# Performance work log

Measured on AMD Instinct MI355X. Metric: run time of the kernel, lower is better.

## Reference

```python
import jax, jax.numpy as jnp
import numpy as np

N = 100000   # nodes
E = 1600000  # edges (avg degree 16)
G = 512      # graphs in batch
IN = 96      # in_channels
H = 128      # hidden_channels
C = 100      # num_classes
ED = 8       # edge_dim
L = 4        # num_layers
EPS_LN = 1e-5


def setup_inputs() -> dict:
    key = jax.random.key(0)
    ks = jax.random.split(key, 24)
    s = 0.05
    d = {
        "x": jax.random.normal(ks[0], (N, IN), jnp.float32),
        "edge_index": jax.random.randint(ks[1], (2, E), 0, N, jnp.int32),
        "batch": jnp.sort(jax.random.randint(ks[2], (N,), 0, G, jnp.int32)),
        "edge_attr": jax.random.normal(ks[3], (E, ED), jnp.float32),
        # edge encoder MLP: Linear(ED,H) -> ReLU -> Linear(H,1)
        "ee_W1": jax.random.normal(ks[4], (ED, H), jnp.float32) * s,
        "ee_b1": jnp.zeros((H,), jnp.float32),
        "ee_W2": jax.random.normal(ks[5], (H, 1), jnp.float32) * s,
        "ee_b2": jnp.zeros((1,), jnp.float32),
        # GCNConv weights (PyG: lin without bias, bias added after aggregation)
        "W0": jax.random.normal(ks[6], (IN, H), jnp.float32) * s,
        "cb0": jnp.zeros((H,), jnp.float32),
        "W1": jax.random.normal(ks[7], (H, H), jnp.float32) * s,
        "cb1": jnp.zeros((H,), jnp.float32),
        "W2": jax.random.normal(ks[8], (H, H), jnp.float32) * s,
        "cb2": jnp.zeros((H,), jnp.float32),
        "W3": jax.random.normal(ks[9], (H, H), jnp.float32) * s,
        "cb3": jnp.zeros((H,), jnp.float32),
        # LayerNorm params
        "g0": jnp.ones((H,), jnp.float32), "be0": jnp.zeros((H,), jnp.float32),
        "g1": jnp.ones((H,), jnp.float32), "be1": jnp.zeros((H,), jnp.float32),
        "g2": jnp.ones((H,), jnp.float32), "be2": jnp.zeros((H,), jnp.float32),
        "g3": jnp.ones((H,), jnp.float32), "be3": jnp.zeros((H,), jnp.float32),
        # residual projection for layer 0 only (IN != H)
        "res_W": jax.random.normal(ks[10], (IN, H), jnp.float32) * s,
        "res_b": jnp.zeros((H,), jnp.float32),
        # head: Linear(2H,H) -> ReLU -> Linear(H,C)
        "hW1": jax.random.normal(ks[11], (2 * H, H), jnp.float32) * s,
        "hb1": jnp.zeros((H,), jnp.float32),
        "hW2": jax.random.normal(ks[12], (H, C), jnp.float32) * s,
        "hb2": jnp.zeros((C,), jnp.float32),
    }
    return d


def _layer_norm(h, g, b):
    mu = jnp.mean(h, axis=-1, keepdims=True)
    var = jnp.mean(jnp.square(h - mu), axis=-1, keepdims=True)
    return g * (h - mu) / jnp.sqrt(var + EPS_LN) + b


def reference(x, edge_index, batch, edge_attr,
              ee_W1, ee_b1, ee_W2, ee_b2,
              W0, cb0, W1, cb1, W2, cb2, W3, cb3,
              g0, be0, g1, be1, g2, be2, g3, be3,
              res_W, res_b, hW1, hb1, hW2, hb2):
    row, col = edge_index[0], edge_index[1]

    # edge weight = softplus(MLP(edge_attr)) + 1e-4  -> [E]
    eh = jax.nn.relu(edge_attr @ ee_W1 + ee_b1)
    ew = jax.nn.softplus((eh @ ee_W2 + ee_b2)[:, 0]) + 1e-4

    # add self loops with weight 1 (PyG GCNConv default)
    loops = jnp.arange(N, dtype=row.dtype)
    row_sl = jnp.concatenate([row, loops])
    col_sl = jnp.concatenate([col, loops])
    ew_sl = jnp.concatenate([ew, jnp.ones((N,), ew.dtype)])

    # symmetric normalization: D^-1/2 A D^-1/2 (deg over target index)
    deg = jax.ops.segment_sum(ew_sl, col_sl, num_segments=N)
    dis = jnp.where(deg > 0, jax.lax.rsqrt(deg), 0.0)
    norm = dis[row_sl] * ew_sl * dis[col_sl]  # [E+N]

    def conv(h, W, b):
        hw = h @ W                                   # [N,H]
        msg = hw[row_sl] * norm[:, None]             # [E+N,H]
        return jax.ops.segment_sum(msg, col_sl, num_segments=N) + b

    Ws = [W0, W1, W2, W3]
    cbs = [cb0, cb1, cb2, cb3]
    gs = [g0, g1, g2, g3]
    bes = [be0, be1, be2, be3]

    hidden = []
    cur = x
    for i in range(L):
        h = conv(cur, Ws[i], cbs[i])
        h = _layer_norm(h, gs[i], bes[i])
        res = cur @ res_W + res_b if i == 0 else cur
        h = jax.nn.relu(h + res)
        # dropout: eval mode -> identity
        hidden.append(h)
        cur = h
    xm = jnp.mean(jnp.stack(hidden, axis=0), axis=0)  # [N,H]

    # meanmax pooling over graphs
    counts = jax.ops.segment_sum(jnp.ones((N,), xm.dtype), batch, num_segments=G)
    gmean = jax.ops.segment_sum(xm, batch, num_segments=G) / jnp.maximum(counts, 1.0)[:, None]
    gmax = jax.ops.segment_max(xm, batch, num_segments=G)
    gmax = jnp.where(jnp.isfinite(gmax), gmax, 0.0)
    g = jnp.concatenate([gmean, gmax], axis=-1)       # [G,2H]

    # head (dropout identity in eval)
    return jax.nn.relu(g @ hW1 + hb1) @ hW2 + hb2     # [G,C]
```

## Files before the change

kernel.cpp:

```cpp
#include <hip/hip_runtime.h>
#include <hip/hip_fp16.h>
#include <math.h>

#define NN 100000
#define EE 1600000
#define GB 512
#define INC 96
#define HH 128
#define CC 100
#define MAXD 64

typedef __bf16 bf16x8 __attribute__((ext_vector_type(8)));
typedef _Float16 f16x8 __attribute__((ext_vector_type(8)));
typedef float f32x4 __attribute__((ext_vector_type(4)));

__global__ __launch_bounds__(256) void k_cast(const float* __restrict__ src, __half* __restrict__ dst, int n4) {
    int i = blockIdx.x * 256 + threadIdx.x;
    if (i >= n4) return;
    float4 v = *(const float4*)&src[(size_t)i * 4];
    __half2 a = __floats2half2_rn(v.x, v.y);
    __half2 b = __floats2half2_rn(v.z, v.w);
    *(__half2*)&dst[(size_t)i * 4]     = a;
    *(__half2*)&dst[(size_t)i * 4 + 2] = b;
}

__global__ __launch_bounds__(256) void k_castT(const float* __restrict__ W, __half* __restrict__ Wt, int K) {
    int idx = blockIdx.x * 256 + threadIdx.x;
    if (idx >= K * 128) return;
    int k = idx >> 7, n = idx & 127;
    Wt[(size_t)n * K + k] = __float2half(W[idx]);
}

__global__ __launch_bounds__(512) void k_prep_w1(const float* __restrict__ W1, __bf16* __restrict__ w1f) {
    int tid = threadIdx.x;
    int t = tid >> 6, lane = tid & 63;
    int ln15 = lane & 15, quad = lane >> 4;
    bf16x8 v = {};
    if (quad == 0) {
#pragma unroll
        for (int j = 0; j < 8; ++j) v[j] = (__bf16)W1[j * 128 + t * 16 + ln15];
    }
    *(bf16x8*)&w1f[(size_t)(t * 64 + lane) * 8] = v;
}

__global__ __launch_bounds__(256) void k_edge_mlp_mfma(
    const float* __restrict__ ea,
    const __bf16* __restrict__ w1f, const float* __restrict__ b1,
    const float* __restrict__ W2, const float* __restrict__ b2,
    float* __restrict__ ew)
{
    __shared__ float sDot[128];
    int tid = threadIdx.x, wv = tid >> 6, lane = tid & 63;
    int ln15 = lane & 15, quad = lane >> 4;
    int ebase = blockIdx.x * 128 + wv * 32;

    bf16x8 bfr[8];
#pragma unroll
    for (int t = 0; t < 8; ++t) bfr[t] = *(const bf16x8*)&w1f[(size_t)(t * 64 + lane) * 8];

    bf16x8 a0 = {}, a1 = {};
    if (quad == 0) {
        const float* p0 = &ea[(size_t)(ebase + ln15) * 8];
        float4 u0 = *(const float4*)p0, u1 = *(const float4*)(p0 + 4);
        a0[0] = (__bf16)u0.x; a0[1] = (__bf16)u0.y; a0[2] = (__bf16)u0.z; a0[3] = (__bf16)u0.w;
        a0[4] = (__bf16)u1.x; a0[5] = (__bf16)u1.y; a0[6] = (__bf16)u1.z; a0[7] = (__bf16)u1.w;
        const float* p1 = &ea[(size_t)(ebase + 16 + ln15) * 8];
        float4 w0 = *(const float4*)p1, w1v = *(const float4*)(p1 + 4);
        a1[0] = (__bf16)w0.x; a1[1] = (__bf16)w0.y; a1[2] = (__bf16)w0.z; a1[3] = (__bf16)w0.w;
        a1[4] = (__bf16)w1v.x; a1[5] = (__bf16)w1v.y; a1[6] = (__bf16)w1v.z; a1[7] = (__bf16)w1v.w;
    }

    f32x4 d0 = {0.f, 0.f, 0.f, 0.f}, d1 = {0.f, 0.f, 0.f, 0.f};
#pragma unroll
    for (int t = 0; t < 8; ++t) {
        f32x4 z = {0.f, 0.f, 0.f, 0.f};
        f32x4 c0 = __builtin_amdgcn_mfma_f32_16x16x32_bf16(a0, bfr[t], z, 0, 0, 0);
        f32x4 c1 = __builtin_amdgcn_mfma_f32_16x16x32_bf16(a1, bfr[t], z, 0, 0, 0);
        int col = t * 16 + ln15;
        float b1v = b1[col], w2v = W2[col];
#pragma unroll
        for (int r = 0; r < 4; ++r) {
            float v0 = fmaxf(c0[r] + b1v, 0.0f);
            float v1 = fmaxf(c1[r] + b1v, 0.0f);
            d0[r] = fmaf(v0, w2v, d0[r]);
            d1[r] = fmaf(v1, w2v, d1[r]);
        }
    }
#pragma unroll
    for (int o = 1; o < 16; o <<= 1) {
#pragma unroll
        for (int r = 0; r < 4; ++r) {
            d0[r] += __shfl_xor(d0[r], o, 64);
            d1[r] += __shfl_xor(d1[r], o, 64);
        }
    }
    if (ln15 == 0) {
#pragma unroll
        for (int r = 0; r < 4; ++r) {
            sDot[wv * 32 + quad * 4 + r]      = d0[r];
            sDot[wv * 32 + 16 + quad * 4 + r] = d1[r];
        }
    }
    __syncthreads();
    if (tid < 128) {
        int e = blockIdx.x * 128 + tid;
        float x = sDot[tid] + b2[0];
        float sp = (x > 20.0f) ? x : log1pf(expf(x));
        ew[e] = sp + 1e-4f;
    }
}

__global__ __launch_bounds__(256) void k_scatter(const int* __restrict__ ei, const float* __restrict__ ew,
                                                 int* __restrict__ cnt, int2* __restrict__ epack, int E) {
    int e = blockIdx.x * 256 + threadIdx.x;
    if (e >= E) return;
    int r = ei[e], c = ei[E + e];
    float w = ew[e];
    int rank = atomicAdd(&cnt[c], 1);
    if (rank < MAXD) epack[(size_t)c * MAXD + rank] = make_int2(r, __float_as_int(w));
}

__global__ __launch_bounds__(256) void k_degk(int* __restrict__ cnt, const int2* __restrict__ epack,
                                              float* __restrict__ dis, int n) {
    int i = blockIdx.x * 256 + threadIdx.x;
    if (i >= n) return;
    int c = cnt[i]; c = c < MAXD ? c : MAXD;
    cnt[i] = c;
    const int2* base = &epack[(size_t)i * MAXD];
    float d = 1.0f;
    for (int k = 0; k < c; ++k) d += __int_as_float(base[k].y);
    dis[i] = rsqrtf(d);
}

__global__ __launch_bounds__(256) void k_norm(const int* __restrict__ cnt, const float* __restrict__ dis,
                                              int2* __restrict__ epack, int n) {
    int wv = threadIdx.x >> 6, lane = threadIdx.x & 63;
    int i = blockIdx.x * 4 + wv;
    if (i >= n) return;
    float dc = dis[i];
    if (lane < cnt[i]) {
        int2 e = epack[(size_t)i * MAXD + lane];
        float wn = dis[e.x] * __int_as_float(e.y) * dc;
        __half h = __float2half(wn);
        __half2 p = __halves2half2(h, h);
        union { __half2 h2; int i32; } u; u.h2 = p;
        epack[(size_t)i * MAXD + lane].y = u.i32;
    }
}

__global__ __launch_bounds__(256) void k_gemm_f16(
    const __half* __restrict__ A, const __half* __restrict__ Bt,
    const float* __restrict__ bias, __half* __restrict__ C, int M, int K)
{
    int tid = threadIdx.x;
    int wv = tid >> 6, lane = tid & 63;
    int ln15 = lane & 15, quad = lane >> 4;
    int m0 = blockIdx.x * 64;
    int n0 = wv * 32;
    f32x4 acc[4][2];
#pragma unroll
    for (int mt = 0; mt < 4; ++mt)
#pragma unroll
        for (int nt = 0; nt < 2; ++nt) acc[mt][nt] = (f32x4){0.f, 0.f, 0.f, 0.f};

    int rowm[4];
#pragma unroll
    for (int mt = 0; mt < 4; ++mt) {
        int r = m0 + mt * 16 + ln15;
        rowm[mt] = r < M ? r : M - 1;
    }
    for (int kc = 0; kc < K; kc += 32) {
        f16x8 af[4], bfr[2];
#pragma unroll
        for (int mt = 0; mt < 4; ++mt)
            af[mt] = *(const f16x8*)&A[(size_t)rowm[mt] * K + kc + quad * 8];
#pragma unroll
        for (int nt = 0; nt < 2; ++nt)
            bfr[nt] = *(const f16x8*)&Bt[(size_t)(n0 + nt * 16 + ln15) * K + kc + quad * 8];
#pragma unroll
        for (int mt = 0; mt < 4; ++mt)
#pragma unroll
            for (int nt = 0; nt < 2; ++nt)
                acc[mt][nt] = __builtin_amdgcn_mfma_f32_16x16x32_f16(af[mt], bfr[nt], acc[mt][nt], 0, 0, 0);
    }
#pragma unroll
    for (int nt = 0; nt < 2; ++nt) {
        int col = n0 + nt * 16 + ln15;
        float bv = bias ? bias[col] : 0.0f;
#pragma unroll
        for (int mt = 0; mt < 4; ++mt) {
#pragma unroll
            for (int r = 0; r < 4; ++r) {
                int row = m0 + mt * 16 + quad * 4 + r;
                if (row < M) C[(size_t)row * 128 + col] = __float2half(acc[mt][nt][r] + bv);
            }
        }
    }
}

__global__ __launch_bounds__(256) void k_agg_ln(
    const __half* __restrict__ hw, const float* __restrict__ dis,
    const int* __restrict__ cnt, const int2* __restrict__ epack,
    const float* __restrict__ cb, const float* __restrict__ gam,
    const float* __restrict__ bet, const __half* __restrict__ res,
    __half* __restrict__ out, int n)
{
    int wv = threadIdx.x >> 6;
    int lane = threadIdx.x & 63;
    int i = blockIdx.x * 4 + wv;
    if (i >= n) return;
    float di = dis[i];
    float sn = di * di;
    __half2 own = *(const __half2*)&hw[(size_t)i * HH + lane * 2];
    __half hsn = __float2half(sn);
    __half2 acc = __hmul2(own, __halves2half2(hsn, hsn));
    int cn = cnt[i];
    const int2* ebase = &epack[(size_t)i * MAXD];
    int k = 0;
    for (; k + 8 <= cn; k += 8) {
        int4 q0 = *(const int4*)&ebase[k];
        int4 q1 = *(const int4*)&ebase[k + 2];
        int4 q2 = *(const int4*)&ebase[k + 4];
        int4 q3 = *(const int4*)&ebase[k + 6];
        __half2 v0 = *(const __half2*)&hw[(size_t)q0.x * HH + lane * 2];
        __half2 v1 = *(const __half2*)&hw[(size_t)q0.z * HH + lane * 2];
        __half2 v2 = *(const __half2*)&hw[(size_t)q1.x * HH + lane * 2];
        __half2 v3 = *(const __half2*)&hw[(size_t)q1.z * HH + lane * 2];
        __half2 v4 = *(const __half2*)&hw[(size_t)q2.x * HH + lane * 2];
        __half2 v5 = *(const __half2*)&hw[(size_t)q2.z * HH + lane * 2];
        __half2 v6 = *(const __half2*)&hw[(size_t)q3.x * HH + lane * 2];
        __half2 v7 = *(const __half2*)&hw[(size_t)q3.z * HH + lane * 2];
        union { int i32; __half2 h2; } w0, w1, w2, w3, w4, w5, w6, w7;
        w0.i32 = q0.y; w1.i32 = q0.w; w2.i32 = q1.y; w3.i32 = q1.w;
        w4.i32 = q2.y; w5.i32 = q2.w; w6.i32 = q3.y; w7.i32 = q3.w;
        acc = __hfma2(v0, w0.h2, acc);
        acc = __hfma2(v1, w1.h2, acc);
        acc = __hfma2(v2, w2.h2, acc);
        acc = __hfma2(v3, w3.h2, acc);
        acc = __hfma2(v4, w4.h2, acc);
        acc = __hfma2(v5, w5.h2, acc);
        acc = __hfma2(v6, w6.h2, acc);
        acc = __hfma2(v7, w7.h2, acc);
    }
    for (; k < cn; ++k) {
        int2 e = ebase[k];
        __half2 v = *(const __half2*)&hw[(size_t)e.x * HH + lane * 2];
        union { int i32; __half2 h2; } w; w.i32 = e.y;
        acc = __hfma2(v, w.h2, acc);
    }
    float2 af = __half22float2(acc);
    float2 cbv = *(const float2*)&cb[lane * 2];
    af.x += cbv.x; af.y += cbv.y;
    float s1 = af.x + af.y;
    float s2 = af.x * af.x + af.y * af.y;
#pragma unroll
    for (int o = 32; o > 0; o >>= 1) {
        s1 += __shfl_xor(s1, o, 64);
        s2 += __shfl_xor(s2, o, 64);
    }
    float mean = s1 * (1.0f / HH);
    float var = fmaxf(s2 * (1.0f / HH) - mean * mean, 0.0f);
    float rstd = rsqrtf(var + 1e-5f);
    float2 gv = *(const float2*)&gam[lane * 2];
    float2 bv = *(const float2*)&bet[lane * 2];
    float2 rv = __half22float2(*(const __half2*)&res[(size_t)i * HH + lane * 2]);
    float hx = fmaxf(fmaf(gv.x, (af.x - mean) * rstd, bv.x) + rv.x, 0.0f);
    float hy = fmaxf(fmaf(gv.y, (af.y - mean) * rstd, bv.y) + rv.y, 0.0f);
    *(__half2*)&out[(size_t)i * HH + lane * 2] = __floats2half2_rn(hx, hy);
}

__global__ __launch_bounds__(128) void k_pool(
    const __half* __restrict__ l0, const __half* __restrict__ l1,
    const __half* __restrict__ l2, const __half* __restrict__ l3,
    const int* __restrict__ batch, float* __restrict__ gbuf, int n)
{
    int g = blockIdx.x, t = threadIdx.x;
    int lo = 0, hi = n;
    while (lo < hi) { int m = (lo + hi) >> 1; if (batch[m] < g) lo = m + 1; else hi = m; }
    int start = lo;
    lo = start; hi = n;
    while (lo < hi) { int m = (lo + hi) >> 1; if (batch[m] < g + 1) lo = m + 1; else hi = m; }
    int end = lo;
    float sum = 0.0f, mx = -INFINITY;
    for (int nd = start; nd < end; ++nd) {
        size_t off = (size_t)nd * HH + t;
        float v = (__half2float(l0[off]) + __half2float(l1[off]) +
                   __half2float(l2[off]) + __half2float(l3[off])) * 0.25f;
        sum += v;
        mx = fmaxf(mx, v);
    }
    int cntg = end - start;
    float mean = sum / fmaxf((float)cntg, 1.0f);
    gbuf[(size_t)g * 256 + t] = mean;
    gbuf[(size_t)g * 256 + 128 + t] = (cntg > 0) ? mx : 0.0f;
}

__global__ __launch_bounds__(128) void k_head(const float* __restrict__ gbuf,
                                              const float* __restrict__ hW1, const float* __restrict__ hb1,
                                              const float* __restrict__ hW2, const float* __restrict__ hb2,
                                              float* __restrict__ out) {
    __shared__ __align__(16) float sg[256];
    __shared__ __align__(16) float sh[128];
    int g = blockIdx.x, t = threadIdx.x;
    sg[t] = gbuf[(size_t)g * 256 + t];
    sg[t + 128] = gbuf[(size_t)g * 256 + 128 + t];
    __syncthreads();
    float h = hb1[t];
    for (int k = 0; k < 256; ++k) h = fmaf(sg[k], hW1[(size_t)k * 128 + t], h);
    sh[t] = fmaxf(h, 0.0f);
    __syncthreads();
    if (t < 100) {
        float o = hb2[t];
        for (int k = 0; k < 128; ++k) o = fmaf(sh[k], hW2[(size_t)k * 100 + t], o);
        out[(size_t)g * 100 + t] = o;
    }
}

extern "C" void kernel_launch(void* const* d_in, const int* in_sizes, int n_in,
                              void* d_out, int out_size, void* d_ws, size_t ws_size,
                              hipStream_t stream) {
    const float* x     = (const float*)d_in[0];
    const int*   ei    = (const int*)d_in[1];
    const int*   batch = (const int*)d_in[2];
    const float* ea    = (const float*)d_in[3];
    const float* eeW1  = (const float*)d_in[4];
    const float* eeb1  = (const float*)d_in[5];
    const float* eeW2  = (const float*)d_in[6];
    const float* eeb2  = (const float*)d_in[7];
    const float* W[4]  = {(const float*)d_in[8], (const float*)d_in[10], (const float*)d_in[12], (const float*)d_in[14]};
    const float* cb[4] = {(const float*)d_in[9], (const float*)d_in[11], (const float*)d_in[13], (const float*)d_in[15]};
    const float* gm[4] = {(const float*)d_in[16], (const float*)d_in[18], (const float*)d_in[20], (const float*)d_in[22]};
    const float* be[4] = {(const float*)d_in[17], (const float*)d_in[19], (const float*)d_in[21], (const float*)d_in[23]};
    const float* resW  = (const float*)d_in[24];
    const float* resb  = (const float*)d_in[25];
    const float* hW1   = (const float*)d_in[26];
    const float* hb1   = (const float*)d_in[27];
    const float* hW2   = (const float*)d_in[28];
    const float* hb2   = (const float*)d_in[29];
    float* out = (float*)d_out;

    char* w = (char*)d_ws;
    auto alloc = [&](size_t bytes) { void* p = w; w += (bytes + 255) & ~(size_t)255; return p; };
    float*  ew     = (float*) alloc((size_t)EE * 4);
    float*  dis    = (float*) alloc((size_t)NN * 4);
    int*    cnt    = (int*)   alloc((size_t)NN * 4);
    int2*   epack  = (int2*)  alloc((size_t)NN * MAXD * 8);
    __half* xb     = (__half*)alloc((size_t)NN * INC * 2);
    __half* hw     = (__half*)alloc((size_t)NN * HH * 2);
    __half* lout[4];
    for (int i = 0; i < 4; ++i) lout[i] = (__half*)alloc((size_t)NN * HH * 2);
    float*  gbuf   = (float*) alloc((size_t)GB * 256 * 4);
    __half* wt0    = (__half*)alloc((size_t)INC * HH * 2);
    __half* wtR    = (__half*)alloc((size_t)INC * HH * 2);
    __half* wt1    = (__half*)alloc((size_t)HH * HH * 2);
    __half* wt2    = (__half*)alloc((size_t)HH * HH * 2);
    __half* wt3    = (__half*)alloc((size_t)HH * HH * 2);
    __bf16* w1f    = (__bf16*)alloc((size_t)8 * 64 * 8 * 2);
    __half* wtc[4] = {wt0, wt1, wt2, wt3};
    __half* res0   = lout[1];

    int nblkN = (NN + 255) / 256;
    int nblkE = (EE + 255) / 256;
    int nblkEdge = EE / 128;
    int nblkGemm = (NN + 63) / 64;
    int nblkCast = (NN * INC / 4 + 255) / 256;
    int nblkT96 = (INC * 128 + 255) / 256;
    int nblkT128 = (HH * 128 + 255) / 256;

    hipMemsetAsync(cnt, 0, (size_t)NN * 4, stream);
    k_cast<<<nblkCast, 256, 0, stream>>>(x, xb, NN * INC / 4);
    k_castT<<<nblkT96, 256, 0, stream>>>(W[0], wt0, INC);
    k_castT<<<nblkT96, 256, 0, stream>>>(resW, wtR, INC);
    k_castT<<<nblkT128, 256, 0, stream>>>(W[1], wt1, HH);
    k_castT<<<nblkT128, 256, 0, stream>>>(W[2], wt2, HH);
    k_castT<<<nblkT128, 256, 0, stream>>>(W[3], wt3, HH);
    k_prep_w1<<<1, 512, 0, stream>>>(eeW1, w1f);
    k_edge_mlp_mfma<<<nblkEdge, 256, 0, stream>>>(ea, w1f, eeb1, eeW2, eeb2, ew);
    k_scatter<<<nblkE, 256, 0, stream>>>(ei, ew, cnt, epack, EE);
    k_degk<<<nblkN, 256, 0, stream>>>(cnt, epack, dis, NN);
    k_norm<<<(NN + 3) / 4, 256, 0, stream>>>(cnt, dis, epack, NN);

    k_gemm_f16<<<nblkGemm, 256, 0, stream>>>(xb, wt0, nullptr, hw, NN, INC);
    k_gemm_f16<<<nblkGemm, 256, 0, stream>>>(xb, wtR, resb, res0, NN, INC);
    k_agg_ln<<<(NN + 3) / 4, 256, 0, stream>>>(hw, dis, cnt, epack,
                                               cb[0], gm[0], be[0], res0, lout[0], NN);
    for (int l = 1; l < 4; ++l) {
        k_gemm_f16<<<nblkGemm, 256, 0, stream>>>(lout[l - 1], wtc[l], nullptr, hw, NN, HH);
        k_agg_ln<<<(NN + 3) / 4, 256, 0, stream>>>(hw, dis, cnt, epack,
                                                   cb[l], gm[l], be[l], lout[l - 1], lout[l], NN);
    }

    k_pool<<<GB, 128, 0, stream>>>(lout[0], lout[1], lout[2], lout[3], batch, gbuf, NN);
    k_head<<<GB, 128, 0, stream>>>(gbuf, hW1, hb1, hW2, hb2, out);
}
```

Before: 916.3 us.

## Replace padded per-node edge slots with compact CSR built via prefix scan

Replaces the fixed 64-slot padded edge storage per destination node with a compact CSR-style layout. Per-node counts are accumulated inside the edge MLP kernel, then turned into offsets by a three-kernel prefix scan, with counts rounded up to even to keep vector loads aligned. A placement kernel fills the edges and accumulates weighted degree with float atomics. This shrinks the edge array and improves locality for the four aggregation passes. In exchange it adds several small launches, a second atomic pass, and degree sums that depend on atomic ordering.

```diff
diff --git a/kernel.cpp b/kernel.cpp
--- a/kernel.cpp
+++ b/kernel.cpp
@@ -8,7 +8,6 @@
 #define INC 96
 #define HH 128
 #define CC 100
-#define MAXD 64
 
 typedef __bf16 bf16x8 __attribute__((ext_vector_type(8)));
 typedef _Float16 f16x8 __attribute__((ext_vector_type(8)));
@@ -47,7 +46,7 @@
     const float* __restrict__ ea,
     const __bf16* __restrict__ w1f, const float* __restrict__ b1,
     const float* __restrict__ W2, const float* __restrict__ b2,
-    float* __restrict__ ew)
+    float* __restrict__ ew, const int* __restrict__ ei, int* __restrict__ cnt)
 {
     __shared__ float sDot[128];
     int tid = threadIdx.x, wv = tid >> 6, lane = tid & 63;
@@ -107,44 +106,82 @@
         float x = sDot[tid] + b2[0];
         float sp = (x > 20.0f) ? x : log1pf(expf(x));
         ew[e] = sp + 1e-4f;
-    }
-}
-
-__global__ __launch_bounds__(256) void k_scatter(const int* __restrict__ ei, const float* __restrict__ ew,
-                                                 int* __restrict__ cnt, int2* __restrict__ epack, int E) {
+        atomicAdd(&cnt[ei[EE + e]], 1);
+    }
+}
+
+__global__ __launch_bounds__(256) void k_scan1(const int* __restrict__ cnt, int* __restrict__ off,
+                                               int* __restrict__ bsum, int n) {
+    __shared__ int s[256];
+    int t = threadIdx.x, i = blockIdx.x * 256 + t;
+    int c = (i < n) ? ((cnt[i] + 1) & ~1) : 0;
+    s[t] = c;
+    __syncthreads();
+#pragma unroll
+    for (int o = 1; o < 256; o <<= 1) {
+        int u = (t >= o) ? s[t - o] : 0;
+        __syncthreads();
+        s[t] += u;
+        __syncthreads();
+    }
+    if (i < n) off[i] = s[t] - c;
+    if (t == 255) bsum[blockIdx.x] = s[255];
+}
+
+__global__ __launch_bounds__(512) void k_scan2(int* __restrict__ bsum, int nb) {
+    __shared__ int s[512];
+    int t = threadIdx.x;
+    int v = (t < nb) ? bsum[t] : 0;
+    s[t] = v;
+    __syncthreads();
+#pragma unroll
+    for (int o = 1; o < 512; o <<= 1) {
+        int u = (t >= o) ? s[t - o] : 0;
+        __syncthreads();
+        s[t] += u;
+        __syncthreads();
+    }
+    if (t < nb) bsum[t] = s[t] - v;
+}
+
+__global__ __launch_bounds__(256) void k_scan3(int* __restrict__ off, const int* __restrict__ bsum, int n) {
+    int i = blockIdx.x * 256 + threadIdx.x;
+    if (i < n) off[i] += bsum[blockIdx.x];
+}
+
+__global__ __launch_bounds__(256) void k_place(const int* __restrict__ ei, const float* __restrict__ ew,
+                                               int* __restrict__ off, float* __restrict__ deg,
+                                               int2* __restrict__ epack, int E) {
     int e = blockIdx.x * 256 + threadIdx.x;
     if (e >= E) return;
     int r = ei[e], c = ei[E + e];
     float w = ew[e];
-    int rank = atomicAdd(&cnt[c], 1);
-    if (rank < MAXD) epack[(size_t)c * MAXD + rank] = make_int2(r, __float_as_int(w));
-}
-
-__global__ __launch_bounds__(256) void k_degk(int* __restrict__ cnt, const int2* __restrict__ epack,
-                                              float* __restrict__ dis, int n) {
+    int pos = atomicAdd(&off[c], 1);
+    epack[pos] = make_int2(r, __float_as_int(w));
+    atomicAdd(&deg[c], w);
+}
+
+__global__ __launch_bounds__(256) void k_dis(const float* __restrict__ deg, float* __restrict__ dis, int n) {
     int i = blockIdx.x * 256 + threadIdx.x;
-    if (i >= n) return;
-    int c = cnt[i]; c = c < MAXD ? c : MAXD;
-    cnt[i] = c;
-    const int2* base = &epack[(size_t)i * MAXD];
-    float d = 1.0f;
-    for (int k = 0; k < c; ++k) d += __int_as_float(base[k].y);
-    dis[i] = rsqrtf(d);
-}
-
-__global__ __launch_bounds__(256) void k_norm(const int* __restrict__ cnt, const float* __restrict__ dis,
+    if (i < n) dis[i] = rsqrtf(1.0f + deg[i]);
+}
+
+__global__ __launch_bounds__(256) void k_norm(const int* __restrict__ cnt, const int* __restrict__ off,
+                                              const float* __restrict__ dis,
                                               int2* __restrict__ epack, int n) {
     int wv = threadIdx.x >> 6, lane = threadIdx.x & 63;
     int i = blockIdx.x * 4 + wv;
     if (i >= n) return;
     float dc = dis[i];
-    if (lane < cnt[i]) {
-        int2 e = epack[(size_t)i * MAXD + lane];
+    int cn = cnt[i];
+    int start = off[i] - cn;
+    for (int k = lane; k < cn; k += 64) {
+        int2 e = epack[(size_t)start + k];
         float wn = dis[e.x] * __int_as_float(e.y) * dc;
         __half h = __float2half(wn);
         __half2 p = __halves2half2(h, h);
         union { __half2 h2; int i32; } u; u.h2 = p;
-        epack[(size_t)i * MAXD + lane].y = u.i32;
+        epack[(size_t)start + k].y = u.i32;
     }
 }
 
@@ -200,7 +237,8 @@
 
 __global__ __launch_bounds__(256) void k_agg_ln(
     const __half* __restrict__ hw, const float* __restrict__ dis,
-    const int* __restrict__ cnt, const int2* __restrict__ epack,
+    const int* __restrict__ cnt, const int* __restrict__ off,
+    const int2* __restrict__ epack,
     const float* __restrict__ cb, const float* __restrict__ gam,
     const float* __restrict__ bet, const __half* __restrict__ res,
     __half* __restrict__ out, int n)
@@ -215,7 +253,7 @@
     __half hsn = __float2half(sn);
     __half2 acc = __hmul2(own, __halves2half2(hsn, hsn));
     int cn = cnt[i];
-    const int2* ebase = &epack[(size_t)i * MAXD];
+    const int2* ebase = &epack[(size_t)(off[i] - cn)];
     int k = 0;
     for (; k + 8 <= cn; k += 8) {
         int4 q0 = *(const int4*)&ebase[k];
@@ -344,7 +382,10 @@
     float*  ew     = (float*) alloc((size_t)EE * 4);
     float*  dis    = (float*) alloc((size_t)NN * 4);
     int*    cnt    = (int*)   alloc((size_t)NN * 4);
-    int2*   epack  = (int2*)  alloc((size_t)NN * MAXD * 8);
+    float*  deg    = (float*) alloc((size_t)NN * 4);
+    int*    off    = (int*)   alloc((size_t)NN * 4);
+    int*    bsum   = (int*)   alloc((size_t)512 * 4);
+    int2*   epack  = (int2*)  alloc((size_t)(EE + NN + 64) * 8);
     __half* xb     = (__half*)alloc((size_t)NN * INC * 2);
     __half* hw     = (__half*)alloc((size_t)NN * HH * 2);
     __half* lout[4];
@@ -368,6 +409,7 @@
     int nblkT128 = (HH * 128 + 255) / 256;
 
     hipMemsetAsync(cnt, 0, (size_t)NN * 4, stream);
+    hipMemsetAsync(deg, 0, (size_t)NN * 4, stream);
     k_cast<<<nblkCast, 256, 0, stream>>>(x, xb, NN * INC / 4);
     k_castT<<<nblkT96, 256, 0, stream>>>(W[0], wt0, INC);
     k_castT<<<nblkT96, 256, 0, stream>>>(resW, wtR, INC);
@@ -375,18 +417,22 @@
     k_castT<<<nblkT128, 256, 0, stream>>>(W[2], wt2, HH);
     k_castT<<<nblkT128, 256, 0, stream>>>(W[3], wt3, HH);
     k_prep_w1<<<1, 512, 0, stream>>>(eeW1, w1f);
-    k_edge_mlp_mfma<<<nblkEdge, 256, 0, stream>>>(ea, w1f, eeb1, eeW2, eeb2, ew);
-    k_scatter<<<nblkE, 256, 0, stream>>>(ei, ew, cnt, epack, EE);
-    k_degk<<<nblkN, 256, 0, stream>>>(cnt, epack, dis, NN);
-    k_norm<<<(NN + 3) / 4, 256, 0, stream>>>(cnt, dis, epack, NN);
+    k_edge_mlp_mfma<<<nblkEdge, 256, 0, stream>>>(ea, w1f, eeb1, eeW2, eeb2, ew, ei, cnt);
+
+    k_scan1<<<nblkN, 256, 0, stream>>>(cnt, off, bsum, NN);
+    k_scan2<<<1, 512, 0, stream>>>(bsum, nblkN);
+    k_scan3<<<nblkN, 256, 0, stream>>>(off, bsum, NN);
+    k_place<<<nblkE, 256, 0, stream>>>(ei, ew, off, deg, epack, EE);
+    k_dis<<<nblkN, 256, 0, stream>>>(deg, dis, NN);
+    k_norm<<<(NN + 3) / 4, 256, 0, stream>>>(cnt, off, dis, epack, NN);
 
     k_gemm_f16<<<nblkGemm, 256, 0, stream>>>(xb, wt0, nullptr, hw, NN, INC);
     k_gemm_f16<<<nblkGemm, 256, 0, stream>>>(xb, wtR, resb, res0, NN, INC);
-    k_agg_ln<<<(NN + 3) / 4, 256, 0, stream>>>(hw, dis, cnt, epack,
+    k_agg_ln<<<(NN + 3) / 4, 256, 0, stream>>>(hw, dis, cnt, off, epack,
                                                cb[0], gm[0], be[0], res0, lout[0], NN);
     for (int l = 1; l < 4; ++l) {
         k_gemm_f16<<<nblkGemm, 256, 0, stream>>>(lout[l - 1], wtc[l], nullptr, hw, NN, HH);
-        k_agg_ln<<<(NN + 3) / 4, 256, 0, stream>>>(hw, dis, cnt, epack,
+        k_agg_ln<<<(NN + 3) / 4, 256, 0, stream>>>(hw, dis, cnt, off, epack,
                                                    cb[l], gm[l], be[l], lout[l - 1], lout[l], NN);
     }
 
```

Result: slower. 996.1 us (+8.7%).

## Pack edge source and fp16 weight into 32-bit word; fuse scatter into edge MLP

Applied to the files above, without the earlier changes.

Each packed edge entry shrinks from 8 bytes to 4, holding the source index in the upper 17 bits and a sign-less fp16 weight in the low 15 bits. The per-edge scatter kernel is folded into the edge-MLP epilogue, so the intermediate edge-weight array and one launch go away. This halves adjacency traffic in the four aggregation passes and in degree and norm prep, at the cost of shift and mask unpacking and dropping the fp16 sign bit. That is safe only because the weights are non-negative and node indices fit in 17 bits.

```diff
diff --git a/kernel.cpp b/kernel.cpp
--- a/kernel.cpp
+++ b/kernel.cpp
@@ -13,6 +13,14 @@
 typedef __bf16 bf16x8 __attribute__((ext_vector_type(8)));
 typedef _Float16 f16x8 __attribute__((ext_vector_type(8)));
 typedef float f32x4 __attribute__((ext_vector_type(4)));
+
+__device__ __forceinline__ float unpack_w_f32(unsigned v) {
+    return __half2float(__ushort_as_half((unsigned short)(v & 0x7FFFu)));
+}
+__device__ __forceinline__ __half2 unpack_w_h2(unsigned v) {
+    __half h = __ushort_as_half((unsigned short)(v & 0x7FFFu));
+    return __halves2half2(h, h);
+}
 
 __global__ __launch_bounds__(256) void k_cast(const float* __restrict__ src, __half* __restrict__ dst, int n4) {
     int i = blockIdx.x * 256 + threadIdx.x;
@@ -47,12 +55,12 @@
     const float* __restrict__ ea,
     const __bf16* __restrict__ w1f, const float* __restrict__ b1,
     const float* __restrict__ W2, const float* __restrict__ b2,
-    float* __restrict__ ew)
+    const int* __restrict__ ei, int* __restrict__ cnt, unsigned* __restrict__ epack)
 {
     __shared__ float sDot[128];
-    int tid = threadIdx.x, wv = tid >> 6, lane = tid & 63;
+    int tid = threadIdx.x, wva = tid >> 6, lane = tid & 63;
     int ln15 = lane & 15, quad = lane >> 4;
-    int ebase = blockIdx.x * 128 + wv * 32;
+    int ebase = blockIdx.x * 128 + wva * 32;
 
     bf16x8 bfr[8];
 #pragma unroll
@@ -97,8 +105,8 @@
     if (ln15 == 0) {
 #pragma unroll
         for (int r = 0; r < 4; ++r) {
-            sDot[wv * 32 + quad * 4 + r]      = d0[r];
-            sDot[wv * 32 + 16 + quad * 4 + r] = d1[r];
+            sDot[wva * 32 + quad * 4 + r]      = d0[r];
+            sDot[wva * 32 + 16 + quad * 4 + r] = d1[r];
         }
     }
     __syncthreads();
@@ -106,45 +114,39 @@
         int e = blockIdx.x * 128 + tid;
         float x = sDot[tid] + b2[0];
         float sp = (x > 20.0f) ? x : log1pf(expf(x));
-        ew[e] = sp + 1e-4f;
-    }
-}
-
-__global__ __launch_bounds__(256) void k_scatter(const int* __restrict__ ei, const float* __restrict__ ew,
-                                                 int* __restrict__ cnt, int2* __restrict__ epack, int E) {
-    int e = blockIdx.x * 256 + threadIdx.x;
-    if (e >= E) return;
-    int r = ei[e], c = ei[E + e];
-    float w = ew[e];
-    int rank = atomicAdd(&cnt[c], 1);
-    if (rank < MAXD) epack[(size_t)c * MAXD + rank] = make_int2(r, __float_as_int(w));
-}
-
-__global__ __launch_bounds__(256) void k_degk(int* __restrict__ cnt, const int2* __restrict__ epack,
+        float wgt = sp + 1e-4f;
+        int r = ei[e], c = ei[EE + e];
+        int rank = atomicAdd(&cnt[c], 1);
+        if (rank < MAXD) {
+            unsigned hb = (unsigned)__half_as_ushort(__float2half(wgt)) & 0x7FFFu;
+            epack[(size_t)c * MAXD + rank] = ((unsigned)r << 15) | hb;
+        }
+    }
+}
+
+__global__ __launch_bounds__(256) void k_degk(int* __restrict__ cnt, const unsigned* __restrict__ epack,
                                               float* __restrict__ dis, int n) {
     int i = blockIdx.x * 256 + threadIdx.x;
     if (i >= n) return;
     int c = cnt[i]; c = c < MAXD ? c : MAXD;
     cnt[i] = c;
-    const int2* base = &epack[(size_t)i * MAXD];
+    const unsigned* base = &epack[(size_t)i * MAXD];
     float d = 1.0f;
-    for (int k = 0; k < c; ++k) d += __int_as_float(base[k].y);
+    for (int k = 0; k < c; ++k) d += unpack_w_f32(base[k]);
     dis[i] = rsqrtf(d);
 }
 
 __global__ __launch_bounds__(256) void k_norm(const int* __restrict__ cnt, const float* __restrict__ dis,
-                                              int2* __restrict__ epack, int n) {
+                                              unsigned* __restrict__ epack, int n) {
     int wv = threadIdx.x >> 6, lane = threadIdx.x & 63;
     int i = blockIdx.x * 4 + wv;
     if (i >= n) return;
     float dc = dis[i];
     if (lane < cnt[i]) {
-        int2 e = epack[(size_t)i * MAXD + lane];
-        float wn = dis[e.x] * __int_as_float(e.y) * dc;
-        __half h = __float2half(wn);
-        __half2 p = __halves2half2(h, h);
-        union { __half2 h2; int i32; } u; u.h2 = p;
-        epack[(size_t)i * MAXD + lane].y = u.i32;
+        unsigned v = epack[(size_t)i * MAXD + lane];
+        float wn = dis[v >> 15] * unpack_w_f32(v) * dc;
+        unsigned hb = (unsigned)__half_as_ushort(__float2half(wn)) & 0x7FFFu;
+        epack[(size_t)i * MAXD + lane] = (v & 0xFFFF8000u) | hb;
     }
 }
 
@@ -200,7 +202,7 @@
 
 __global__ __launch_bounds__(256) void k_agg_ln(
     const __half* __restrict__ hw, const float* __restrict__ dis,
-    const int* __restrict__ cnt, const int2* __restrict__ epack,
+    const int* __restrict__ cnt, const unsigned* __restrict__ epack,
     const float* __restrict__ cb, const float* __restrict__ gam,
     const float* __restrict__ bet, const __half* __restrict__ res,
     __half* __restrict__ out, int n)
@@ -215,38 +217,32 @@
     __half hsn = __float2half(sn);
     __half2 acc = __hmul2(own, __halves2half2(hsn, hsn));
     int cn = cnt[i];
-    const int2* ebase = &epack[(size_t)i * MAXD];
+    const unsigned* ebase = &epack[(size_t)i * MAXD];
     int k = 0;
     for (; k + 8 <= cn; k += 8) {
-        int4 q0 = *(const int4*)&ebase[k];
-        int4 q1 = *(const int4*)&ebase[k + 2];
-        int4 q2 = *(const int4*)&ebase[k + 4];
-        int4 q3 = *(const int4*)&ebase[k + 6];
-        __half2 v0 = *(const __half2*)&hw[(size_t)q0.x * HH + lane * 2];
-        __half2 v1 = *(const __half2*)&hw[(size_t)q0.z * HH + lane * 2];
-        __half2 v2 = *(const __half2*)&hw[(size_t)q1.x * HH + lane * 2];
-        __half2 v3 = *(const __half2*)&hw[(size_t)q1.z * HH + lane * 2];
-        __half2 v4 = *(const __half2*)&hw[(size_t)q2.x * HH + lane * 2];
-        __half2 v5 = *(const __half2*)&hw[(size_t)q2.z * HH + lane * 2];
-        __half2 v6 = *(const __half2*)&hw[(size_t)q3.x * HH + lane * 2];
-        __half2 v7 = *(const __half2*)&hw[(size_t)q3.z * HH + lane * 2];
-        union { int i32; __half2 h2; } w0, w1, w2, w3, w4, w5, w6, w7;
-        w0.i32 = q0.y; w1.i32 = q0.w; w2.i32 = q1.y; w3.i32 = q1.w;
-        w4.i32 = q2.y; w5.i32 = q2.w; w6.i32 = q3.y; w7.i32 = q3.w;
-        acc = __hfma2(v0, w0.h2, acc);
-        acc = __hfma2(v1, w1.h2, acc);
-        acc = __hfma2(v2, w2.h2, acc);
-        acc = __hfma2(v3, w3.h2, acc);
-        acc = __hfma2(v4, w4.h2, acc);
-        acc = __hfma2(v5, w5.h2, acc);
-        acc = __hfma2(v6, w6.h2, acc);
-        acc = __hfma2(v7, w7.h2, acc);
+        uint4 q0 = *(const uint4*)&ebase[k];
+        uint4 q1 = *(const uint4*)&ebase[k + 4];
+        __half2 v0 = *(const __half2*)&hw[(size_t)(q0.x >> 15) * HH + lane * 2];
+        __half2 v1 = *(const __half2*)&hw[(size_t)(q0.y >> 15) * HH + lane * 2];
+        __half2 v2 = *(const __half2*)&hw[(size_t)(q0.z >> 15) * HH + lane * 2];
+        __half2 v3 = *(const __half2*)&hw[(size_t)(q0.w >> 15) * HH + lane * 2];
+        __half2 v4 = *(const __half2*)&hw[(size_t)(q1.x >> 15) * HH + lane * 2];
+        __half2 v5 = *(const __half2*)&hw[(size_t)(q1.y >> 15) * HH + lane * 2];
+        __half2 v6 = *(const __half2*)&hw[(size_t)(q1.z >> 15) * HH + lane * 2];
+        __half2 v7 = *(const __half2*)&hw[(size_t)(q1.w >> 15) * HH + lane * 2];
+        acc = __hfma2(v0, unpack_w_h2(q0.x), acc);
+        acc = __hfma2(v1, unpack_w_h2(q0.y), acc);
+        acc = __hfma2(v2, unpack_w_h2(q0.z), acc);
+        acc = __hfma2(v3, unpack_w_h2(q0.w), acc);
+        acc = __hfma2(v4, unpack_w_h2(q1.x), acc);
+        acc = __hfma2(v5, unpack_w_h2(q1.y), acc);
+        acc = __hfma2(v6, unpack_w_h2(q1.z), acc);
+        acc = __hfma2(v7, unpack_w_h2(q1.w), acc);
     }
     for (; k < cn; ++k) {
-        int2 e = ebase[k];
-        __half2 v = *(const __half2*)&hw[(size_t)e.x * HH + lane * 2];
-        union { int i32; __half2 h2; } w; w.i32 = e.y;
-        acc = __hfma2(v, w.h2, acc);
+        unsigned e = ebase[k];
+        __half2 v = *(const __half2*)&hw[(size_t)(e >> 15) * HH + lane * 2];
+        acc = __hfma2(v, unpack_w_h2(e), acc);
     }
     float2 af = __half22float2(acc);
     float2 cbv = *(const float2*)&cb[lane * 2];
@@ -341,26 +337,24 @@
 
     char* w = (char*)d_ws;
     auto alloc = [&](size_t bytes) { void* p = w; w += (bytes + 255) & ~(size_t)255; return p; };
-    float*  ew     = (float*) alloc((size_t)EE * 4);
-    float*  dis    = (float*) alloc((size_t)NN * 4);
-    int*    cnt    = (int*)   alloc((size_t)NN * 4);
-    int2*   epack  = (int2*)  alloc((size_t)NN * MAXD * 8);
-    __half* xb     = (__half*)alloc((size_t)NN * INC * 2);
-    __half* hw     = (__half*)alloc((size_t)NN * HH * 2);
-    __half* lout[4];
+    float*    dis    = (float*)   alloc((size_t)NN * 4);
+    int*      cnt    = (int*)     alloc((size_t)NN * 4);
+    unsigned* epack  = (unsigned*)alloc((size_t)NN * MAXD * 4);
+    __half*   xb     = (__half*)  alloc((size_t)NN * INC * 2);
+    __half*   hw     = (__half*)  alloc((size_t)NN * HH * 2);
+    __half*   lout[4];
     for (int i = 0; i < 4; ++i) lout[i] = (__half*)alloc((size_t)NN * HH * 2);
-    float*  gbuf   = (float*) alloc((size_t)GB * 256 * 4);
-    __half* wt0    = (__half*)alloc((size_t)INC * HH * 2);
-    __half* wtR    = (__half*)alloc((size_t)INC * HH * 2);
-    __half* wt1    = (__half*)alloc((size_t)HH * HH * 2);
-    __half* wt2    = (__half*)alloc((size_t)HH * HH * 2);
-    __half* wt3    = (__half*)alloc((size_t)HH * HH * 2);
-    __bf16* w1f    = (__bf16*)alloc((size_t)8 * 64 * 8 * 2);
-    __half* wtc[4] = {wt0, wt1, wt2, wt3};
-    __half* res0   = lout[1];
+    float*    gbuf   = (float*)   alloc((size_t)GB * 256 * 4);
+    __half*   wt0    = (__half*)  alloc((size_t)INC * HH * 2);
+    __half*   wtR    = (__half*)  alloc((size_t)INC * HH * 2);
+    __half*   wt1    = (__half*)  alloc((size_t)HH * HH * 2);
+    __half*   wt2    = (__half*)  alloc((size_t)HH * HH * 2);
+    __half*   wt3    = (__half*)  alloc((size_t)HH * HH * 2);
+    __bf16*   w1f    = (__bf16*)  alloc((size_t)8 * 64 * 8 * 2);
+    __half*   wtc[4] = {wt0, wt1, wt2, wt3};
+    __half*   res0   = lout[1];
 
     int nblkN = (NN + 255) / 256;
-    int nblkE = (EE + 255) / 256;
     int nblkEdge = EE / 128;
     int nblkGemm = (NN + 63) / 64;
     int nblkCast = (NN * INC / 4 + 255) / 256;
@@ -375,8 +369,7 @@
     k_castT<<<nblkT128, 256, 0, stream>>>(W[2], wt2, HH);
     k_castT<<<nblkT128, 256, 0, stream>>>(W[3], wt3, HH);
     k_prep_w1<<<1, 512, 0, stream>>>(eeW1, w1f);
-    k_edge_mlp_mfma<<<nblkEdge, 256, 0, stream>>>(ea, w1f, eeb1, eeW2, eeb2, ew);
-    k_scatter<<<nblkE, 256, 0, stream>>>(ei, ew, cnt, epack, EE);
+    k_edge_mlp_mfma<<<nblkEdge, 256, 0, stream>>>(ea, w1f, eeb1, eeW2, eeb2, ei, cnt, epack);
     k_degk<<<nblkN, 256, 0, stream>>>(cnt, epack, dis, NN);
     k_norm<<<(NN + 3) / 4, 256, 0, stream>>>(cnt, dis, epack, NN);
 
```

New measurement: 854.3 us. -6.8%, faster.
